# Kernel tuning notes

Hardware: AMD Instinct MI355X
Metric: run time of the kernel (lower is better)

## Reference

```python
import jax, jax.numpy as jnp
import numpy as np

B, S, E, H = 1, 2048, 512, 8
D = E // H
N = B * S
WIN_HALF = 32  # attention_window 64 -> +/-32
ALPHA = 0.1
LN_EPS = 1e-12
NEG_INF = -1e9


def _build_window_edges():
    # windowed graph: dst i attends to src j with |i-j| <= WIN_HALF, within each batch block
    i = np.arange(S)
    offs = np.arange(-WIN_HALF, WIN_HALF + 1)
    src = i[:, None] + offs[None, :]
    dst = np.broadcast_to(i[:, None], src.shape)
    valid = (src >= 0) & (src < S)
    src, dst = src[valid], dst[valid]
    srcs, dsts = [], []
    for b in range(B):
        srcs.append(src + b * S)
        dsts.append(dst + b * S)
    return (np.concatenate(srcs).astype(np.int32),
            np.concatenate(dsts).astype(np.int32))


def setup_inputs() -> dict:
    key = jax.random.key(0)
    ks = jax.random.split(key, 12)
    sc = 1.0 / np.sqrt(E)
    src_np, dst_np = _build_window_edges()
    return {
        "hidden_states": jax.random.normal(ks[0], (B, S, E), dtype=jnp.float32),
        "attention_mask": jnp.zeros((B, S), dtype=jnp.float32),
        "edge_src": jnp.asarray(src_np),
        "edge_dst": jnp.asarray(dst_np),
        "Wq": jax.random.normal(ks[1], (E, E), dtype=jnp.float32) * sc,
        "bq": jnp.zeros((E,), dtype=jnp.float32),
        "Wk": jax.random.normal(ks[2], (E, E), dtype=jnp.float32) * sc,
        "bk": jnp.zeros((E,), dtype=jnp.float32),
        "Wv": jax.random.normal(ks[3], (E, E), dtype=jnp.float32) * sc,
        "bv": jnp.zeros((E,), dtype=jnp.float32),
        "Wo": jax.random.normal(ks[4], (E, E), dtype=jnp.float32) * sc,
        "bo": jnp.zeros((E,), dtype=jnp.float32),
        "ln_g": jnp.ones((E,), dtype=jnp.float32),
        "ln_b": jnp.zeros((E,), dtype=jnp.float32),
    }


def reference(hidden_states, attention_mask, edge_src, edge_dst,
              Wq, bq, Wk, bk, Wv, bv, Wo, bo, ln_g, ln_b):
    x = hidden_states  # (B,S,E); node ordering n = b*S + s (matches torch reshape)
    q = ((x @ Wq + bq) / jnp.sqrt(jnp.asarray(D, x.dtype))).reshape(N, H, D)
    k = (x @ Wk + bk).reshape(N, H, D)
    v = (x @ Wv + bv).reshape(N, H, D)

    mask = (attention_mask >= 0).reshape(N)  # bool per node

    # u_dot_v('k','q','score'): per-edge, per-head dot product
    score = jnp.einsum('ehd,ehd->eh', k[edge_src], q[edge_dst])  # (Eg,H)
    score = jnp.where(mask[edge_src][:, None], score, NEG_INF)

    # edge_softmax over incoming edges of each destination node
    smax = jax.ops.segment_max(score, edge_dst, num_segments=N)
    p = jnp.exp(score - smax[edge_dst])
    denom = jax.ops.segment_sum(p, edge_dst, num_segments=N)
    p = p / denom[edge_dst]  # (Eg,H)

    # 5 diffusion steps: h <- A h, blended with residual v (dropout off in eval)
    h = v
    for _ in range(5):
        m = h[edge_src] * p[:, :, None]                      # u_mul_e
        h = jax.ops.segment_sum(m, edge_dst, num_segments=N)  # sum('m','h')
        h = (1.0 - ALPHA) * h + ALPHA * v

    attn = h.reshape(B, S, E)

    # DiffuserSelfOutput: dense -> residual add -> LayerNorm
    y = attn @ Wo + bo + hidden_states
    mu = y.mean(-1, keepdims=True)
    var = ((y - mu) ** 2).mean(-1, keepdims=True)
    out = (y - mu) * jax.lax.rsqrt(var + LN_EPS) * ln_g + ln_b
    return out
```

## Files before the change

### kernel.cpp

```cpp
#include <hip/hip_runtime.h>
#include <math.h>

#define S_LEN 2048
#define E_DIM 512
#define NE (S_LEN * E_DIM)
#define H_NUM 8
#define WH 32
#define NOFF 65
#define PROW (H_NUM * NOFF)
#define PN (S_LEN * PROW)

typedef float f32x4 __attribute__((ext_vector_type(4)));
typedef short short8 __attribute__((ext_vector_type(8)));

__device__ __forceinline__ unsigned short f2bf(float f) {
    union { float f; unsigned u; } cv; cv.f = f;
    unsigned u = cv.u;
    u += 0x7fffu + ((u >> 16) & 1u);
    return (unsigned short)(u >> 16);
}
__device__ __forceinline__ unsigned pk2(float x, float y) {
    return (unsigned)f2bf(x) | ((unsigned)f2bf(y) << 16);
}

#define LGKM_BARRIER() do {                                   \
    __builtin_amdgcn_sched_barrier(0);                        \
    asm volatile("s_waitcnt lgkmcnt(0)" ::: "memory");        \
    __builtin_amdgcn_s_barrier();                             \
    __builtin_amdgcn_sched_barrier(0);                        \
} while (0)

__device__ __forceinline__ void mfma_gemm_f32(
    const float* __restrict__ A, const float* __restrict__ W,
    const float* __restrict__ bias, float* __restrict__ C,
    float scale, int m0, int n0)
{
    __shared__ unsigned short As[2][64 * 40];
    __shared__ unsigned short Bs[2][64 * 40];
    const int tid = threadIdx.x;
    const int lane = tid & 63, wave = tid >> 6;
    const int quad = lane >> 4, l16 = lane & 15;
    const int wr = (wave >> 1) * 32, wc = (wave & 1) * 32;
    const int ar = tid >> 2, ac = (tid & 3) * 8;
    const int bn = tid & 63, bk0 = (tid >> 6) * 8;

    f32x4 acc00 = {0.f,0.f,0.f,0.f}, acc01 = acc00, acc10 = acc00, acc11 = acc00;

    const float* Arow = A + (size_t)(m0 + ar) * E_DIM;

    float4 a0r[2], a1r[2];
    float  br[2][8];

#define QLOAD(s_, i_) do {                                                    \
        int kk_ = (i_) * 32;                                                  \
        a0r[s_] = *(const float4*)(Arow + kk_ + ac);                          \
        a1r[s_] = *(const float4*)(Arow + kk_ + ac + 4);                      \
        _Pragma("unroll")                                                     \
        for (int j_ = 0; j_ < 8; ++j_)                                        \
            br[s_][j_] = W[(size_t)(kk_ + bk0 + j_) * E_DIM + n0 + bn];       \
    } while (0)

#define QPACK(s_, b_) do {                                                    \
        uint4 ap_;                                                            \
        ap_.x = pk2(a0r[s_].x, a0r[s_].y); ap_.y = pk2(a0r[s_].z, a0r[s_].w); \
        ap_.z = pk2(a1r[s_].x, a1r[s_].y); ap_.w = pk2(a1r[s_].z, a1r[s_].w); \
        *(uint4*)(&As[b_][0] + ar * 40 + ac) = ap_;                           \
        uint4 bp_;                                                            \
        bp_.x = pk2(br[s_][0], br[s_][1]); bp_.y = pk2(br[s_][2], br[s_][3]); \
        bp_.z = pk2(br[s_][4], br[s_][5]); bp_.w = pk2(br[s_][6], br[s_][7]); \
        *(uint4*)(&Bs[b_][0] + bn * 40 + bk0) = bp_;                          \
    } while (0)

    QLOAD(0, 0);
    QPACK(0, 0);
    QLOAD(1, 1);
    LGKM_BARRIER();

#pragma unroll
    for (int it = 0; it < 16; ++it) {
        if (it < 14) QLOAD(it & 1, it + 2);

        const unsigned short* Ab = &As[it & 1][0];
        const unsigned short* Bb = &Bs[it & 1][0];
        short8 fa0 = *(const short8*)(Ab + (wr + l16) * 40 + quad * 8);
        short8 fa1 = *(const short8*)(Ab + (wr + 16 + l16) * 40 + quad * 8);
        short8 fb0 = *(const short8*)(Bb + (wc + l16) * 40 + quad * 8);
        short8 fb1 = *(const short8*)(Bb + (wc + 16 + l16) * 40 + quad * 8);
        acc00 = __builtin_amdgcn_mfma_f32_16x16x32_bf16(fa0, fb0, acc00, 0, 0, 0);
        acc01 = __builtin_amdgcn_mfma_f32_16x16x32_bf16(fa0, fb1, acc01, 0, 0, 0);
        acc10 = __builtin_amdgcn_mfma_f32_16x16x32_bf16(fa1, fb0, acc10, 0, 0, 0);
        acc11 = __builtin_amdgcn_mfma_f32_16x16x32_bf16(fa1, fb1, acc11, 0, 0, 0);

        if (it < 15) {
            QPACK((it + 1) & 1, (it + 1) & 1);
            LGKM_BARRIER();
        }
    }
#undef QLOAD
#undef QPACK

#pragma unroll
    for (int mi = 0; mi < 2; ++mi) {
#pragma unroll
        for (int ni = 0; ni < 2; ++ni) {
            f32x4 a = (mi == 0) ? ((ni == 0) ? acc00 : acc01)
                                : ((ni == 0) ? acc10 : acc11);
            int n = n0 + wc + ni * 16 + l16;
            float bval = bias[n];
#pragma unroll
            for (int r = 0; r < 4; ++r) {
                int m = m0 + wr + mi * 16 + quad * 4 + r;
                C[(size_t)m * E_DIM + n] = (a[r] + bval) * scale;
            }
        }
    }
}

__global__ __launch_bounds__(256)
void qkv_gemm(const float* __restrict__ x,
              const float* __restrict__ Wq, const float* __restrict__ bq,
              const float* __restrict__ Wk, const float* __restrict__ bk,
              const float* __restrict__ Wv, const float* __restrict__ bv,
              float* __restrict__ q, float* __restrict__ k, float* __restrict__ v)
{
    const float* W; const float* b; float* o; float sc;
    if (blockIdx.z == 0)      { W = Wq; b = bq; o = q; sc = 0.125f; }
    else if (blockIdx.z == 1) { W = Wk; b = bk; o = k; sc = 1.0f; }
    else                      { W = Wv; b = bv; o = v; sc = 1.0f; }
    mfma_gemm_f32(x, W, b, o, sc, blockIdx.y * 64, blockIdx.x * 64);
}

#define SDN 32
__global__ __launch_bounds__(256)
void scores_d1(const float* __restrict__ q, const float* __restrict__ k,
               const float* __restrict__ v, const float* __restrict__ amask,
               float* __restrict__ P, float* __restrict__ hA)
{
    const int i0 = blockIdx.x * SDN;
    const int h  = blockIdx.y;
    const int tid = threadIdx.x;
    __shared__ float ks[96 * 68];
    __shared__ float am[96];
    __shared__ float ps[SDN * NOFF];

    for (int e = tid; e < 96 * 16; e += 256) {
        int lr = e >> 4, c4 = e & 15;
        int j = i0 - WH + lr;
        int jc = min(max(j, 0), S_LEN - 1);
        *(float4*)(ks + lr * 68 + c4 * 4) =
            *(const float4*)(k + (size_t)jc * E_DIM + h * 64 + c4 * 4);
    }
    if (tid < 96) {
        int j = i0 - WH + tid;
        am[tid] = (j >= 0 && j < S_LEN) ? amask[j] : -1.0f;
    }

    const int dst = tid >> 3;
    const int og  = tid & 7;
    float4 qreg[16];
    {
        const float4* qrow = (const float4*)(q + (size_t)(i0 + dst) * E_DIM + h * 64);
#pragma unroll
        for (int t = 0; t < 16; ++t) qreg[t] = qrow[t];
    }
    __syncthreads();

    float sreg[9];
#pragma unroll
    for (int t = 0; t < 9; ++t) sreg[t] = -INFINITY;
#pragma unroll
    for (int t = 0; t < 9; ++t) {
        int off = og + 8 * t;
        if (off > 64) break;
        int j = i0 + dst + off - WH;
        if (j >= 0 && j < S_LEN) {
            int lr = dst + off;
            const float4* kr = (const float4*)(ks + lr * 68);
            float acc = 0.f;
#pragma unroll
            for (int u = 0; u < 16; ++u) {
                float4 a = qreg[u], bb = kr[u];
                acc += a.x * bb.x + a.y * bb.y + a.z * bb.z + a.w * bb.w;
            }
            sreg[t] = (am[lr] >= 0.f) ? acc : -1e9f;
        }
    }
    __syncthreads();

    for (int e = tid; e < 96 * 16; e += 256) {
        int lr = e >> 4, c4 = e & 15;
        int j = i0 - WH + lr;
        int jc = min(max(j, 0), S_LEN - 1);
        *(float4*)(ks + lr * 68 + c4 * 4) =
            *(const float4*)(v + (size_t)jc * E_DIM + h * 64 + c4 * 4);
    }

    float mx = sreg[0];
#pragma unroll
    for (int t = 1; t < 9; ++t) mx = fmaxf(mx, sreg[t]);
#pragma unroll
    for (int o = 1; o < 8; o <<= 1) mx = fmaxf(mx, __shfl_xor(mx, o, 64));
    float dn = 0.f;
#pragma unroll
    for (int t = 0; t < 9; ++t) {
        sreg[t] = expf(sreg[t] - mx);
        dn += sreg[t];
    }
#pragma unroll
    for (int o = 1; o < 8; o <<= 1) dn += __shfl_xor(dn, o, 64);
    float rinv = 1.f / dn;
#pragma unroll
    for (int t = 0; t < 9; ++t) {
        int off = og + 8 * t;
        if (off > 64) break;
        float pv = sreg[t] * rinv;
        P[(size_t)(i0 + dst) * PROW + h * NOFF + off] = pv;
        ps[dst * NOFF + off] = pv;
    }
    __syncthreads();

    {
        const int ci = tid & 15;
        const int ob = (tid >> 4) * 2;
        float4 a0 = {0,0,0,0}, a1 = a0;
        for (int lr = ob; lr < ob + 66; ++lr) {
            float4 hval = *(const float4*)(ks + lr * 68 + ci * 4);
            int o0 = lr - ob;
            if (o0 <= 64) {
                float p = ps[ob * NOFF + o0];
                a0.x += p * hval.x; a0.y += p * hval.y; a0.z += p * hval.z; a0.w += p * hval.w;
            }
            int o1 = o0 - 1;
            if ((unsigned)o1 <= 64u) {
                float p = ps[(ob + 1) * NOFF + o1];
                a1.x += p * hval.x; a1.y += p * hval.y; a1.z += p * hval.z; a1.w += p * hval.w;
            }
        }
#pragma unroll
        for (int r = 0; r < 2; ++r) {
            float4 a = r ? a1 : a0;
            float4 vv = *(const float4*)(ks + (WH + ob + r) * 68 + ci * 4);
            float4 o;
            o.x = 0.9f * a.x + 0.1f * vv.x;
            o.y = 0.9f * a.y + 0.1f * vv.y;
            o.z = 0.9f * a.z + 0.1f * vv.z;
            o.w = 0.9f * a.w + 0.1f * vv.w;
            *(float4*)(hA + (size_t)(i0 + ob + r) * E_DIM + h * 64 + ci * 4) = o;
        }
    }
}

__global__ __launch_bounds__(512)
void diffuse4m(const float* __restrict__ hin, const float* __restrict__ v,
               const float* __restrict__ P, unsigned short* __restrict__ h5b)
{
    __shared__ unsigned short inT[64 * 328];
    __shared__ unsigned short m1T[64 * 264];
    __shared__ unsigned short ps[256 * 66];
    unsigned short* m2T = inT;
    unsigned short* m3T = m1T;
    const int i0 = blockIdx.x * 64;
    const int h  = blockIdx.y;
    const int c0 = h * 64;
    const int tid  = threadIdx.x;
    const int lane = tid & 63, wave = tid >> 6;
    const int quad = lane >> 4, l16 = lane & 15;

    for (int e = tid; e < 160 * 16; e += 512) {
        int rp = (e >> 4) * 2, c4 = (e & 15) * 4;
        int ja = min(max(i0 - 128 + rp,     0), S_LEN - 1);
        int jb = min(max(i0 - 128 + rp + 1, 0), S_LEN - 1);
        float4 ha = *(const float4*)(hin + (size_t)ja * E_DIM + c0 + c4);
        float4 hb = *(const float4*)(hin + (size_t)jb * E_DIM + c0 + c4);
        *(unsigned*)(inT + (c4 + 0) * 328 + rp) = pk2(ha.x, hb.x);
        *(unsigned*)(inT + (c4 + 1) * 328 + rp) = pk2(ha.y, hb.y);
        *(unsigned*)(inT + (c4 + 2) * 328 + rp) = pk2(ha.z, hb.z);
        *(unsigned*)(inT + (c4 + 3) * 328 + rp) = pk2(ha.w, hb.w);
    }
    for (int e = tid; e < 256 * 33; e += 512) {
        int mr = e / 33, t = e - mr * 33;
        int jc = min(max(i0 - 96 + mr, 0), S_LEN - 1);
        const float* pr = P + (size_t)jc * PROW + h * NOFF;
        if (t < 32)
            *(unsigned*)(ps + mr * 66 + t * 2) = pk2(pr[t * 2], pr[t * 2 + 1]);
        else
            ps[mr * 66 + 64] = f2bf(pr[64]);
    }
    __syncthreads();

#pragma unroll
    for (int uu = 0; uu < 4; ++uu) {
        int u = wave + uu * 8;
        int mtb = (u >> 1) * 16;
        int ntb = (u & 1) * 32;
        f32x4 a0 = {0.f,0.f,0.f,0.f}, a1 = a0;
        int ks0 = mtb >> 5;
        const int m = mtb + l16;
#pragma unroll
        for (int t = 0; t < 3; ++t) {
            int k0q = (ks0 + t) * 32 + quad * 8;
            short8 fa;
#pragma unroll
            for (int j = 0; j < 8; ++j) {
                int idx = k0q + j - m;
                int idc = min(max(idx, 0), 64);
                unsigned short pv = ps[m * 66 + idc];
                fa[j] = ((unsigned)idx <= 64u) ? (short)pv : (short)0;
            }
            short8 fb0 = *(const short8*)(inT + (ntb + l16) * 328 + k0q);
            short8 fb1 = *(const short8*)(inT + (ntb + 16 + l16) * 328 + k0q);
            a0 = __builtin_amdgcn_mfma_f32_16x16x32_bf16(fa, fb0, a0, 0, 0, 0);
            a1 = __builtin_amdgcn_mfma_f32_16x16x32_bf16(fa, fb1, a1, 0, 0, 0);
        }
#pragma unroll
        for (int nt = 0; nt < 2; ++nt) {
            f32x4 a = nt ? a1 : a0;
            int n = ntb + nt * 16 + l16;
            float o[4];
#pragma unroll
            for (int r = 0; r < 4; ++r) {
                int gm = min(max(i0 - 96 + mtb + quad * 4 + r, 0), S_LEN - 1);
                o[r] = 0.9f * a[r] + 0.1f * v[(size_t)gm * E_DIM + c0 + n];
            }
            *(unsigned*)(m1T + n * 264 + mtb + quad * 4)     = pk2(o[0], o[1]);
            *(unsigned*)(m1T + n * 264 + mtb + quad * 4 + 2) = pk2(o[2], o[3]);
        }
    }
    __syncthreads();

#pragma unroll
    for (int uu = 0; uu < 3; ++uu) {
        int u = wave + uu * 8;
        int mtb = (u >> 1) * 16;
        int ntb = (u & 1) * 32;
        f32x4 a0 = {0.f,0.f,0.f,0.f}, a1 = a0;
        int ks0 = mtb >> 5;
        const int m = mtb + l16;
#pragma unroll
        for (int t = 0; t < 3; ++t) {
            int k0q = (ks0 + t) * 32 + quad * 8;
            short8 fa;
#pragma unroll
            for (int j = 0; j < 8; ++j) {
                int idx = k0q + j - m;
                int idc = min(max(idx, 0), 64);
                unsigned short pv = ps[(m + 32) * 66 + idc];
                fa[j] = ((unsigned)idx <= 64u) ? (short)pv : (short)0;
            }
            short8 fb0 = *(const short8*)(m1T + (ntb + l16) * 264 + k0q);
            short8 fb1 = *(const short8*)(m1T + (ntb + 16 + l16) * 264 + k0q);
            a0 = __builtin_amdgcn_mfma_f32_16x16x32_bf16(fa, fb0, a0, 0, 0, 0);
            a1 = __builtin_amdgcn_mfma_f32_16x16x32_bf16(fa, fb1, a1, 0, 0, 0);
        }
#pragma unroll
        for (int nt = 0; nt < 2; ++nt) {
            f32x4 a = nt ? a1 : a0;
            int n = ntb + nt * 16 + l16;
            float o[4];
#pragma unroll
            for (int r = 0; r < 4; ++r) {
                int gm = min(max(i0 - 64 + mtb + quad * 4 + r, 0), S_LEN - 1);
                o[r] = 0.9f * a[r] + 0.1f * v[(size_t)gm * E_DIM + c0 + n];
            }
            *(unsigned*)(m2T + n * 200 + mtb + quad * 4)     = pk2(o[0], o[1]);
            *(unsigned*)(m2T + n * 200 + mtb + quad * 4 + 2) = pk2(o[2], o[3]);
        }
    }
    __syncthreads();

#pragma unroll
    for (int uu = 0; uu < 2; ++uu) {
        int u = wave + uu * 8;
        int mtb = (u >> 1) * 16;
        int ntb = (u & 1) * 32;
        f32x4 a0 = {0.f,0.f,0.f,0.f}, a1 = a0;
        int ks0 = mtb >> 5;
        const int m = mtb + l16;
#pragma unroll
        for (int t = 0; t < 3; ++t) {
            int k0q = (ks0 + t) * 32 + quad * 8;
            short8 fa;
#pragma unroll
            for (int j = 0; j < 8; ++j) {
                int idx = k0q + j - m;
                int idc = min(max(idx, 0), 64);
                unsigned short pv = ps[(m + 64) * 66 + idc];
                fa[j] = ((unsigned)idx <= 64u) ? (short)pv : (short)0;
            }
            short8 fb0 = *(const short8*)(m2T + (ntb + l16) * 200 + k0q);
            short8 fb1 = *(const short8*)(m2T + (ntb + 16 + l16) * 200 + k0q);
            a0 = __builtin_amdgcn_mfma_f32_16x16x32_bf16(fa, fb0, a0, 0, 0, 0);
            a1 = __builtin_amdgcn_mfma_f32_16x16x32_bf16(fa, fb1, a1, 0, 0, 0);
        }
#pragma unroll
        for (int nt = 0; nt < 2; ++nt) {
            f32x4 a = nt ? a1 : a0;
            int n = ntb + nt * 16 + l16;
            float o[4];
#pragma unroll
            for (int r = 0; r < 4; ++r) {
                int gm = min(max(i0 - 32 + mtb + quad * 4 + r, 0), S_LEN - 1);
                o[r] = 0.9f * a[r] + 0.1f * v[(size_t)gm * E_DIM + c0 + n];
            }
            *(unsigned*)(m3T + n * 136 + mtb + quad * 4)     = pk2(o[0], o[1]);
            *(unsigned*)(m3T + n * 136 + mtb + quad * 4 + 2) = pk2(o[2], o[3]);
        }
    }
    __syncthreads();

    {
        int u = wave;
        int mtb = (u >> 1) * 16;
        int ntb = (u & 1) * 32;
        f32x4 a0 = {0.f,0.f,0.f,0.f}, a1 = a0;
        int ks0 = mtb >> 5;
        const int m = mtb + l16;
#pragma unroll
        for (int t = 0; t < 3; ++t) {
            int k0q = (ks0 + t) * 32 + quad * 8;
            short8 fa;
#pragma unroll
            for (int j = 0; j < 8; ++j) {
                int idx = k0q + j - m;
                int idc = min(max(idx, 0), 64);
                unsigned short pv = ps[(m + 96) * 66 + idc];
                fa[j] = ((unsigned)idx <= 64u) ? (short)pv : (short)0;
            }
            short8 fb0 = *(const short8*)(m3T + (ntb + l16) * 136 + k0q);
            short8 fb1 = *(const short8*)(m3T + (ntb + 16 + l16) * 136 + k0q);
            a0 = __builtin_amdgcn_mfma_f32_16x16x32_bf16(fa, fb0, a0, 0, 0, 0);
            a1 = __builtin_amdgcn_mfma_f32_16x16x32_bf16(fa, fb1, a1, 0, 0, 0);
        }
#pragma unroll
        for (int nt = 0; nt < 2; ++nt) {
            f32x4 a = nt ? a1 : a0;
            int n = ntb + nt * 16 + l16;
#pragma unroll
            for (int r = 0; r < 4; ++r) {
                int gm = i0 + mtb + quad * 4 + r;
                float vv = v[(size_t)gm * E_DIM + c0 + n];
                h5b[(size_t)gm * E_DIM + c0 + n] = f2bf(0.9f * a[r] + 0.1f * vv);
            }
        }
    }
}

__global__ __launch_bounds__(512)
void oln5(const unsigned short* __restrict__ h5b, const float* __restrict__ Wo,
          const float* __restrict__ bo, const float* __restrict__ x,
          const float* __restrict__ g, const float* __restrict__ lb,
          float* __restrict__ out)
{
    __shared__ unsigned short Bs2[2][512 * 40];
    __shared__ float rsum[8][16], rsq[8][16];
    const int tid = threadIdx.x;
    const int lane = tid & 63, wave = tid >> 6;
    const int quad = lane >> 4, l16 = lane & 15;
    const int m0 = blockIdx.x * 16;
    const int n = tid;

    short8 far_[16];
#pragma unroll
    for (int t = 0; t < 16; ++t)
        far_[t] = *(const short8*)(h5b + (size_t)(m0 + l16) * E_DIM + t * 32 + quad * 8);

    {
        float w0[32];
#pragma unroll
        for (int j = 0; j < 32; ++j)
            w0[j] = Wo[(size_t)j * E_DIM + n];
#pragma unroll
        for (int t = 0; t < 4; ++t) {
            uint4 bp;
            bp.x = pk2(w0[t*8+0], w0[t*8+1]); bp.y = pk2(w0[t*8+2], w0[t*8+3]);
            bp.z = pk2(w0[t*8+4], w0[t*8+5]); bp.w = pk2(w0[t*8+6], w0[t*8+7]);
            *(uint4*)(&Bs2[0][0] + n * 40 + t * 8) = bp;
        }
    }
    LGKM_BARRIER();

    f32x4 acc[4];
#pragma unroll
    for (int t = 0; t < 4; ++t) acc[t] = (f32x4){0.f,0.f,0.f,0.f};

#pragma unroll
    for (int it = 0; it < 16; ++it) {
        float wn[32];
        if (it < 15) {
#pragma unroll
            for (int j = 0; j < 32; ++j)
                wn[j] = Wo[(size_t)((it + 1) * 32 + j) * E_DIM + n];
        }

#pragma unroll
        for (int nt = 0; nt < 4; ++nt) {
            short8 fb = *(const short8*)(&Bs2[it & 1][0] +
                                         (wave * 64 + nt * 16 + l16) * 40 + quad * 8);
            acc[nt] = __builtin_amdgcn_mfma_f32_16x16x32_bf16(far_[it], fb, acc[nt], 0, 0, 0);
        }

        if (it < 15) {
#pragma unroll
            for (int t = 0; t < 4; ++t) {
                uint4 bp;
                bp.x = pk2(wn[t*8+0], wn[t*8+1]); bp.y = pk2(wn[t*8+2], wn[t*8+3]);
                bp.z = pk2(wn[t*8+4], wn[t*8+5]); bp.w = pk2(wn[t*8+6], wn[t*8+7]);
                *(uint4*)(&Bs2[(it + 1) & 1][0] + n * 40 + t * 8) = bp;
            }
            LGKM_BARRIER();
        }
    }

    float s[4] = {0.f,0.f,0.f,0.f}, s2[4] = {0.f,0.f,0.f,0.f};
#pragma unroll
    for (int nt = 0; nt < 4; ++nt) {
        int nc = wave * 64 + nt * 16 + l16;
        float bv = bo[nc];
#pragma unroll
        for (int r = 0; r < 4; ++r) {
            int m = m0 + quad * 4 + r;
            float vl = acc[nt][r] + bv + x[(size_t)m * E_DIM + nc];
            acc[nt][r] = vl;
            s[r] += vl; s2[r] += vl * vl;
        }
    }
#pragma unroll
    for (int o = 1; o < 16; o <<= 1) {
#pragma unroll
        for (int r = 0; r < 4; ++r) {
            s[r]  += __shfl_xor(s[r], o, 64);
            s2[r] += __shfl_xor(s2[r], o, 64);
        }
    }
    if (l16 == 0) {
#pragma unroll
        for (int r = 0; r < 4; ++r) {
            rsum[wave][quad * 4 + r] = s[r];
            rsq[wave][quad * 4 + r]  = s2[r];
        }
    }
    __syncthreads();
    float mu[4], rs[4];
#pragma unroll
    for (int r = 0; r < 4; ++r) {
        int rl = quad * 4 + r;
        float tot = 0.f, tot2 = 0.f;
#pragma unroll
        for (int w = 0; w < 8; ++w) { tot += rsum[w][rl]; tot2 += rsq[w][rl]; }
        float m_ = tot * (1.f / 512.f);
        float var = tot2 * (1.f / 512.f) - m_ * m_;
        mu[r] = m_; rs[r] = rsqrtf(var + 1e-12f);
    }
#pragma unroll
    for (int nt = 0; nt < 4; ++nt) {
        int nc = wave * 64 + nt * 16 + l16;
        float gv = g[nc], bbv = lb[nc];
#pragma unroll
        for (int r = 0; r < 4; ++r) {
            int m = m0 + quad * 4 + r;
            out[(size_t)m * E_DIM + nc] = (acc[nt][r] - mu[r]) * rs[r] * gv + bbv;
        }
    }
}

extern "C" void kernel_launch(void* const* d_in, const int* in_sizes, int n_in,
                              void* d_out, int out_size, void* d_ws, size_t ws_size,
                              hipStream_t stream)
{
    const float* x     = (const float*)d_in[0];
    const float* amask = (const float*)d_in[1];
    const float* Wq = (const float*)d_in[4];
    const float* bq = (const float*)d_in[5];
    const float* Wk = (const float*)d_in[6];
    const float* bk = (const float*)d_in[7];
    const float* Wv = (const float*)d_in[8];
    const float* bv = (const float*)d_in[9];
    const float* Wo = (const float*)d_in[10];
    const float* bo = (const float*)d_in[11];
    const float* lng = (const float*)d_in[12];
    const float* lnb = (const float*)d_in[13];
    float* out = (float*)d_out;

    float* ws = (float*)d_ws;
    float* q  = ws;
    float* k  = ws + (size_t)NE;
    float* v  = ws + (size_t)2 * NE;
    float* P  = ws + (size_t)3 * NE;
    float* hA = ws + (size_t)3 * NE + PN;
    unsigned short* h5b = (unsigned short*)(ws + (size_t)4 * NE + PN);

    qkv_gemm<<<dim3(8, 32, 3), 256, 0, stream>>>(x, Wq, bq, Wk, bk, Wv, bv, q, k, v);

    scores_d1<<<dim3(64, 8), 256, 0, stream>>>(q, k, v, amask, P, hA);

    diffuse4m<<<dim3(32, 8), 512, 0, stream>>>(hA, v, P, h5b);

    oln5<<<128, 512, 0, stream>>>(h5b, Wo, bo, x, lng, lnb, out);
}
```

Before: 164.4 us.

## Store P and hA in bf16 and read band A-fragments as vector loads

scores_d1 now writes the softmax probabilities and the first diffusion result as bf16 rather than fp32, which halves the intermediate traffic into diffuse4m and removes the conversion work there. diffuse4m stores each P row in a zero-padded shared buffer, shifted so that the banded A fragment for the MFMA becomes a single aligned short8 load instead of eight clamped, masked scalar loads. This costs more LDS for the padded buffer plus a zero-fill pass and an extra barrier.

```diff
diff --git a/kernel.cpp b/kernel.cpp
--- a/kernel.cpp
+++ b/kernel.cpp
@@ -134,7 +134,7 @@
 __global__ __launch_bounds__(256)
 void scores_d1(const float* __restrict__ q, const float* __restrict__ k,
                const float* __restrict__ v, const float* __restrict__ amask,
-               float* __restrict__ P, float* __restrict__ hA)
+               unsigned short* __restrict__ Pb, unsigned short* __restrict__ hAb)
 {
     const int i0 = blockIdx.x * SDN;
     const int h  = blockIdx.y;
@@ -214,7 +214,7 @@
         int off = og + 8 * t;
         if (off > 64) break;
         float pv = sreg[t] * rinv;
-        P[(size_t)(i0 + dst) * PROW + h * NOFF + off] = pv;
+        Pb[(size_t)(i0 + dst) * PROW + h * NOFF + off] = f2bf(pv);
         ps[dst * NOFF + off] = pv;
     }
     __syncthreads();
@@ -240,23 +240,23 @@
         for (int r = 0; r < 2; ++r) {
             float4 a = r ? a1 : a0;
             float4 vv = *(const float4*)(ks + (WH + ob + r) * 68 + ci * 4);
-            float4 o;
-            o.x = 0.9f * a.x + 0.1f * vv.x;
-            o.y = 0.9f * a.y + 0.1f * vv.y;
-            o.z = 0.9f * a.z + 0.1f * vv.z;
-            o.w = 0.9f * a.w + 0.1f * vv.w;
-            *(float4*)(hA + (size_t)(i0 + ob + r) * E_DIM + h * 64 + ci * 4) = o;
+            ushort4 o4;
+            o4.x = f2bf(0.9f * a.x + 0.1f * vv.x);
+            o4.y = f2bf(0.9f * a.y + 0.1f * vv.y);
+            o4.z = f2bf(0.9f * a.z + 0.1f * vv.z);
+            o4.w = f2bf(0.9f * a.w + 0.1f * vv.w);
+            *(ushort4*)(hAb + (size_t)(i0 + ob + r) * E_DIM + h * 64 + ci * 4) = o4;
         }
     }
 }
 
 __global__ __launch_bounds__(512)
-void diffuse4m(const float* __restrict__ hin, const float* __restrict__ v,
-               const float* __restrict__ P, unsigned short* __restrict__ h5b)
+void diffuse4m(const unsigned short* __restrict__ hAb, const float* __restrict__ v,
+               const unsigned short* __restrict__ Pb, unsigned short* __restrict__ h5b)
 {
     __shared__ unsigned short inT[64 * 328];
     __shared__ unsigned short m1T[64 * 264];
-    __shared__ unsigned short ps[256 * 66];
+    __shared__ unsigned short ps2[256 * 136];
     unsigned short* m2T = inT;
     unsigned short* m3T = m1T;
     const int i0 = blockIdx.x * 64;
@@ -266,27 +266,35 @@
     const int lane = tid & 63, wave = tid >> 6;
     const int quad = lane >> 4, l16 = lane & 15;
 
+    for (int e = tid; e < 256 * 68; e += 512)
+        ((unsigned*)ps2)[e] = 0u;
+
     for (int e = tid; e < 160 * 16; e += 512) {
         int rp = (e >> 4) * 2, c4 = (e & 15) * 4;
         int ja = min(max(i0 - 128 + rp,     0), S_LEN - 1);
         int jb = min(max(i0 - 128 + rp + 1, 0), S_LEN - 1);
-        float4 ha = *(const float4*)(hin + (size_t)ja * E_DIM + c0 + c4);
-        float4 hb = *(const float4*)(hin + (size_t)jb * E_DIM + c0 + c4);
-        *(unsigned*)(inT + (c4 + 0) * 328 + rp) = pk2(ha.x, hb.x);
-        *(unsigned*)(inT + (c4 + 1) * 328 + rp) = pk2(ha.y, hb.y);
-        *(unsigned*)(inT + (c4 + 2) * 328 + rp) = pk2(ha.z, hb.z);
-        *(unsigned*)(inT + (c4 + 3) * 328 + rp) = pk2(ha.w, hb.w);
-    }
-    for (int e = tid; e < 256 * 33; e += 512) {
-        int mr = e / 33, t = e - mr * 33;
-        int jc = min(max(i0 - 96 + mr, 0), S_LEN - 1);
-        const float* pr = P + (size_t)jc * PROW + h * NOFF;
-        if (t < 32)
-            *(unsigned*)(ps + mr * 66 + t * 2) = pk2(pr[t * 2], pr[t * 2 + 1]);
-        else
-            ps[mr * 66 + 64] = f2bf(pr[64]);
-    }
-    __syncthreads();
+        ushort4 ha = *(const ushort4*)(hAb + (size_t)ja * E_DIM + c0 + c4);
+        ushort4 hb = *(const ushort4*)(hAb + (size_t)jb * E_DIM + c0 + c4);
+        *(unsigned*)(inT + (c4 + 0) * 328 + rp) = (unsigned)ha.x | ((unsigned)hb.x << 16);
+        *(unsigned*)(inT + (c4 + 1) * 328 + rp) = (unsigned)ha.y | ((unsigned)hb.y << 16);
+        *(unsigned*)(inT + (c4 + 2) * 328 + rp) = (unsigned)ha.z | ((unsigned)hb.z << 16);
+        *(unsigned*)(inT + (c4 + 3) * 328 + rp) = (unsigned)ha.w | ((unsigned)hb.w << 16);
+    }
+    __syncthreads();
+
+    for (int it = 0; it < 32; ++it) {
+        int row = wave + it * 8;
+        int jc = min(max(i0 - 96 + row, 0), S_LEN - 1);
+        const unsigned short* src = Pb + (size_t)jc * PROW + h * NOFF;
+        unsigned short* dst = ps2 + row * 136 + 32 + (row & 7);
+        dst[lane] = src[lane];
+        if (lane == 0) dst[64] = src[64];
+    }
+    __syncthreads();
+
+#define BAND_FA(roff_)                                                        \
+    *(const short8*)(ps2 + (size_t)(m + (roff_)) * 136 + 32 +                 \
+                     ((m + (roff_)) & 7) + (k0q - m))
 
 #pragma unroll
     for (int uu = 0; uu < 4; ++uu) {
@@ -299,14 +307,7 @@
 #pragma unroll
         for (int t = 0; t < 3; ++t) {
             int k0q = (ks0 + t) * 32 + quad * 8;
-            short8 fa;
-#pragma unroll
-            for (int j = 0; j < 8; ++j) {
-                int idx = k0q + j - m;
-                int idc = min(max(idx, 0), 64);
-                unsigned short pv = ps[m * 66 + idc];
-                fa[j] = ((unsigned)idx <= 64u) ? (short)pv : (short)0;
-            }
+            short8 fa = BAND_FA(0);
             short8 fb0 = *(const short8*)(inT + (ntb + l16) * 328 + k0q);
             short8 fb1 = *(const short8*)(inT + (ntb + 16 + l16) * 328 + k0q);
             a0 = __builtin_amdgcn_mfma_f32_16x16x32_bf16(fa, fb0, a0, 0, 0, 0);
@@ -339,14 +340,7 @@
 #pragma unroll
         for (int t = 0; t < 3; ++t) {
             int k0q = (ks0 + t) * 32 + quad * 8;
-            short8 fa;
-#pragma unroll
-            for (int j = 0; j < 8; ++j) {
-                int idx = k0q + j - m;
-                int idc = min(max(idx, 0), 64);
-                unsigned short pv = ps[(m + 32) * 66 + idc];
-                fa[j] = ((unsigned)idx <= 64u) ? (short)pv : (short)0;
-            }
+            short8 fa = BAND_FA(32);
             short8 fb0 = *(const short8*)(m1T + (ntb + l16) * 264 + k0q);
             short8 fb1 = *(const short8*)(m1T + (ntb + 16 + l16) * 264 + k0q);
             a0 = __builtin_amdgcn_mfma_f32_16x16x32_bf16(fa, fb0, a0, 0, 0, 0);
@@ -379,14 +373,7 @@
 #pragma unroll
         for (int t = 0; t < 3; ++t) {
             int k0q = (ks0 + t) * 32 + quad * 8;
-            short8 fa;
-#pragma unroll
-            for (int j = 0; j < 8; ++j) {
-                int idx = k0q + j - m;
-                int idc = min(max(idx, 0), 64);
-                unsigned short pv = ps[(m + 64) * 66 + idc];
-                fa[j] = ((unsigned)idx <= 64u) ? (short)pv : (short)0;
-            }
+            short8 fa = BAND_FA(64);
             short8 fb0 = *(const short8*)(m2T + (ntb + l16) * 200 + k0q);
             short8 fb1 = *(const short8*)(m2T + (ntb + 16 + l16) * 200 + k0q);
             a0 = __builtin_amdgcn_mfma_f32_16x16x32_bf16(fa, fb0, a0, 0, 0, 0);
@@ -418,14 +405,7 @@
 #pragma unroll
         for (int t = 0; t < 3; ++t) {
             int k0q = (ks0 + t) * 32 + quad * 8;
-            short8 fa;
-#pragma unroll
-            for (int j = 0; j < 8; ++j) {
-                int idx = k0q + j - m;
-                int idc = min(max(idx, 0), 64);
-                unsigned short pv = ps[(m + 96) * 66 + idc];
-                fa[j] = ((unsigned)idx <= 64u) ? (short)pv : (short)0;
-            }
+            short8 fa = BAND_FA(96);
             short8 fb0 = *(const short8*)(m3T + (ntb + l16) * 136 + k0q);
             short8 fb1 = *(const short8*)(m3T + (ntb + 16 + l16) * 136 + k0q);
             a0 = __builtin_amdgcn_mfma_f32_16x16x32_bf16(fa, fb0, a0, 0, 0, 0);
@@ -443,6 +423,7 @@
             }
         }
     }
+#undef BAND_FA
 }
 
 __global__ __launch_bounds__(512)
@@ -585,15 +566,15 @@
     float* q  = ws;
     float* k  = ws + (size_t)NE;
     float* v  = ws + (size_t)2 * NE;
-    float* P  = ws + (size_t)3 * NE;
-    float* hA = ws + (size_t)3 * NE + PN;
-    unsigned short* h5b = (unsigned short*)(ws + (size_t)4 * NE + PN);
+    unsigned short* Pb  = (unsigned short*)(ws + (size_t)3 * NE);
+    unsigned short* hAb = Pb + (size_t)PN;
+    unsigned short* h5b = hAb + (size_t)NE;
 
     qkv_gemm<<<dim3(8, 32, 3), 256, 0, stream>>>(x, Wq, bq, Wk, bk, Wv, bv, q, k, v);
 
-    scores_d1<<<dim3(64, 8), 256, 0, stream>>>(q, k, v, amask, P, hA);
-
-    diffuse4m<<<dim3(32, 8), 512, 0, stream>>>(hA, v, P, h5b);
+    scores_d1<<<dim3(64, 8), 256, 0, stream>>>(q, k, v, amask, Pb, hAb);
+
+    diffuse4m<<<dim3(32, 8), 512, 0, stream>>>(hAb, v, Pb, h5b);
 
     oln5<<<128, 512, 0, stream>>>(h5b, Wo, bo, x, lng, lnb, out);
 }
```

Measured after the change: 155.1 us. 5.7% less time.
